# Performance work log

Hardware: AMD Instinct MI355X
Metric: run time of the kernel (lower is better)

## Reference

```python
import jax, jax.numpy as jnp
import numpy as np

BS, TS, H = 16, 2048, 1024
MT_LEN = TS // 2  # static split point; matches first_sentence_mask built in setup_inputs
SCALE = 1.0 / float(np.sqrt(H))
NEG = -10000.0


def masked_average(x, mask):
    # x: (bs, ts, h), mask: (bs, ts) -> (bs, h)
    m = mask[..., None].astype(x.dtype)
    return (x * m).sum(1) / m.sum(1)


def setup_inputs() -> dict:
    key = jax.random.key(0)
    ks = jax.random.split(key, 8)
    hidden_states = jax.random.normal(ks[0], (BS, TS, H), jnp.float32)
    embeddings = jax.random.normal(ks[1], (BS, TS, H), jnp.float32)
    attention_mask = jnp.ones((BS, TS), jnp.int32)
    first_sentence_mask = jnp.concatenate(
        [jnp.ones((BS, MT_LEN), jnp.int32), jnp.zeros((BS, TS - MT_LEN), jnp.int32)], axis=1)
    first_piece_mask = jnp.ones((BS, TS), jnp.int32)  # unused (aggregation='none')
    s = 1.0 / float(np.sqrt(H))
    Wq = jax.random.normal(ks[2], (H, H), jnp.float32) * s
    bq = jnp.zeros((H,), jnp.float32)
    Wk = jax.random.normal(ks[3], (H, H), jnp.float32) * s
    bk = jnp.zeros((H,), jnp.float32)
    Wv = jax.random.normal(ks[4], (H, H), jnp.float32) * s
    bv = jnp.zeros((H,), jnp.float32)
    return dict(hidden_states=hidden_states, embeddings=embeddings,
                attention_mask=attention_mask, first_sentence_mask=first_sentence_mask,
                first_piece_mask=first_piece_mask,
                Wq=Wq, bq=bq, Wk=Wk, bk=bk, Wv=Wv, bv=bv)


def reference(hidden_states, embeddings, attention_mask, first_sentence_mask,
              first_piece_mask, Wq, bq, Wk, bk, Wv, bv):
    # alpha_merge < 0, squared_attn=False, kv_rep='embeddings', alpha=1.0 (softmax)
    kv_rep = embeddings
    hidden_states_avg = masked_average(hidden_states, attention_mask)   # (bs, h)
    q = hidden_states_avg @ Wq.T + bq                                   # (bs, h)
    k = kv_rep @ Wk.T + bk                                              # (bs, ts, h)
    v = kv_rep @ Wv.T + bv                                              # (bs, ts, h)
    scores = jnp.einsum('bh,bth->bt', q, k) * SCALE                     # (bs, ts)
    scores = jnp.where(attention_mask.astype(bool), scores, NEG)
    probas = jax.nn.softmax(scores, axis=-1)                            # (bs, ts)
    combined_summary = jnp.einsum('bt,bth->bh', probas, v)              # (bs, h)
    # separate_mt_and_src on probas (static split at MT_LEN)
    mt_mask = attention_mask[:, :MT_LEN] * first_sentence_mask[:, :MT_LEN]
    src_mask = attention_mask[:, MT_LEN:] * (1 - first_sentence_mask[:, MT_LEN:])
    mt_probas = probas[:, :MT_LEN] * mt_mask.astype(probas.dtype)
    src_probas = probas[:, MT_LEN:] * src_mask.astype(probas.dtype)
    return combined_summary, mt_probas, src_probas
```

## Files before the change

### kernel.cpp

```cpp
#include <hip/hip_runtime.h>

#define BS 16
#define TS 2048
#define H 1024
#define MT_LEN 1024
#define NCHUNK 64
#define CHUNK_T (TS / NCHUNK)
#define SCALE 0.03125f
#define NEG -10000.0f

__global__ __launch_bounds__(256)
void k1_hidden_partial(const float* __restrict__ hs,
                       const int* __restrict__ am,
                       float* __restrict__ pA) {
    const int c = blockIdx.x, b = blockIdx.y;
    const int tid = threadIdx.x;
    const int h4 = tid * 4;
    __shared__ float ms[CHUNK_T];
    if (tid < CHUNK_T) ms[tid] = (float)am[b * TS + c * CHUNK_T + tid];
    __syncthreads();
    const float* base = hs + ((size_t)(b * TS + c * CHUNK_T)) * H + h4;
    float4 acc = {0.f, 0.f, 0.f, 0.f};
#pragma unroll 4
    for (int t = 0; t < CHUNK_T; ++t) {
        float m = ms[t];
        float4 v = *(const float4*)(base + (size_t)t * H);
        acc.x += m * v.x; acc.y += m * v.y; acc.z += m * v.z; acc.w += m * v.w;
    }
    *(float4*)(pA + ((size_t)(b * NCHUNK + c)) * H + h4) = acc;
}

__global__ __launch_bounds__(256)
void k3_q(const float* __restrict__ pA, const int* __restrict__ am,
          const float* __restrict__ Wq, const float* __restrict__ bq,
          float* __restrict__ q) {
    const int ic = blockIdx.x, b = blockIdx.y;
    const int tid = threadIdx.x;
    __shared__ float avs[H];
    __shared__ float red[256];
    int s = 0;
    for (int t = tid; t < TS; t += 256) s += am[b * TS + t];
    red[tid] = (float)s;
    __syncthreads();
    for (int o = 128; o > 0; o >>= 1) { if (tid < o) red[tid] += red[tid + o]; __syncthreads(); }
    const float inv = 1.0f / red[0];
    const int h4 = tid * 4;
    float4 acc = {0.f, 0.f, 0.f, 0.f};
    for (int c = 0; c < NCHUNK; ++c) {
        float4 v = *(const float4*)(pA + ((size_t)(b * NCHUNK + c)) * H + h4);
        acc.x += v.x; acc.y += v.y; acc.z += v.z; acc.w += v.w;
    }
    avs[h4] = acc.x * inv; avs[h4 + 1] = acc.y * inv;
    avs[h4 + 2] = acc.z * inv; avs[h4 + 3] = acc.w * inv;
    __syncthreads();
    const int i = ic * 256 + tid;
    const float* row = Wq + (size_t)i * H;
    float a = 0.f;
    for (int j = 0; j < H; j += 4) {
        float4 w = *(const float4*)(row + j);
        a += w.x * avs[j] + w.y * avs[j + 1] + w.z * avs[j + 2] + w.w * avs[j + 3];
    }
    q[b * H + i] = a + bq[i];
}

__global__ __launch_bounds__(256)
void k4_qk(const float* __restrict__ q, const float* __restrict__ Wk,
           const float* __restrict__ bk, float* __restrict__ qk,
           float* __restrict__ qbk) {
    const int jc = blockIdx.x, b = blockIdx.y;
    const int tid = threadIdx.x;
    __shared__ float qs[H];
    for (int i = tid; i < H; i += 256) qs[i] = q[b * H + i];
    __syncthreads();
    const int j = jc * 256 + tid;
    float acc = 0.f;
    for (int i = 0; i < H; ++i) acc += qs[i] * Wk[(size_t)i * H + j];
    qk[b * H + j] = acc;
    if (jc == 0) {
        __shared__ float red[256];
        float s = 0.f;
        for (int i = tid; i < H; i += 256) s += qs[i] * bk[i];
        red[tid] = s;
        __syncthreads();
        for (int o = 128; o > 0; o >>= 1) { if (tid < o) red[tid] += red[tid + o]; __syncthreads(); }
        if (tid == 0) qbk[b] = red[0];
    }
}

__global__ __launch_bounds__(256)
void k5_scores(const float* __restrict__ emb, const int* __restrict__ am,
               const float* __restrict__ qk, const float* __restrict__ qbk,
               float* __restrict__ scores) {
    const int c = blockIdx.x, b = blockIdx.y;
    const int tid = threadIdx.x;
    const int wave = tid >> 6, lane = tid & 63;
    __shared__ float qks[H];
    for (int j = tid; j < H; j += 256) qks[j] = qk[b * H + j];
    __syncthreads();
    const float qb = qbk[b];
    const int tbase = c * CHUNK_T + wave * (CHUNK_T / 4);
    for (int tt = 0; tt < CHUNK_T / 4; ++tt) {
        const int t = tbase + tt;
        const float* e = emb + ((size_t)(b * TS + t)) * H;
        float acc = 0.f;
#pragma unroll
        for (int u = 0; u < 4; ++u) {
            const int j = lane * 4 + u * 256;
            float4 v = *(const float4*)(e + j);
            acc += v.x * qks[j] + v.y * qks[j + 1] + v.z * qks[j + 2] + v.w * qks[j + 3];
        }
#pragma unroll
        for (int o = 32; o > 0; o >>= 1) acc += __shfl_xor(acc, o);
        if (lane == 0) {
            scores[b * TS + t] = (am[b * TS + t] != 0) ? (acc + qb) * SCALE : NEG;
        }
    }
}

__global__ __launch_bounds__(256)
void k6_softmax(const float* __restrict__ scores, const int* __restrict__ am,
                const int* __restrict__ fs, float* __restrict__ probas,
                float* __restrict__ out) {
    const int b = blockIdx.x;
    const int tid = threadIdx.x;
    __shared__ float red[256];
    float local[8];
    float mx = -3.4e38f;
#pragma unroll
    for (int u = 0; u < 8; ++u) {
        local[u] = scores[b * TS + tid + u * 256];
        mx = fmaxf(mx, local[u]);
    }
    red[tid] = mx;
    __syncthreads();
    for (int o = 128; o > 0; o >>= 1) { if (tid < o) red[tid] = fmaxf(red[tid], red[tid + o]); __syncthreads(); }
    mx = red[0];
    __syncthreads();
    float sum = 0.f;
#pragma unroll
    for (int u = 0; u < 8; ++u) { local[u] = __expf(local[u] - mx); sum += local[u]; }
    red[tid] = sum;
    __syncthreads();
    for (int o = 128; o > 0; o >>= 1) { if (tid < o) red[tid] += red[tid + o]; __syncthreads(); }
    const float inv = 1.0f / red[0];
#pragma unroll
    for (int u = 0; u < 8; ++u) {
        const int t = tid + u * 256;
        const float p = local[u] * inv;
        probas[b * TS + t] = p;
        const int a = am[b * TS + t];
        const int f = fs[b * TS + t];
        if (t < MT_LEN)
            out[BS * H + b * MT_LEN + t] = p * (float)(a * f);
        else
            out[BS * H + BS * MT_LEN + b * (TS - MT_LEN) + (t - MT_LEN)] = p * (float)(a * (1 - f));
    }
}

__global__ __launch_bounds__(256)
void k7_wemb(const float* __restrict__ emb, const float* __restrict__ probas,
             float* __restrict__ pC) {
    const int c = blockIdx.x, b = blockIdx.y;
    const int tid = threadIdx.x;
    __shared__ float ps[CHUNK_T];
    if (tid < CHUNK_T) ps[tid] = probas[b * TS + c * CHUNK_T + tid];
    __syncthreads();
    const int h4 = tid * 4;
    const float* base = emb + ((size_t)(b * TS + c * CHUNK_T)) * H + h4;
    float4 acc = {0.f, 0.f, 0.f, 0.f};
#pragma unroll 4
    for (int t = 0; t < CHUNK_T; ++t) {
        const float p = ps[t];
        float4 v = *(const float4*)(base + (size_t)t * H);
        acc.x += p * v.x; acc.y += p * v.y; acc.z += p * v.z; acc.w += p * v.w;
    }
    *(float4*)(pC + ((size_t)(b * NCHUNK + c)) * H + h4) = acc;
}

__global__ __launch_bounds__(256)
void k8_combined(const float* __restrict__ pC, const float* __restrict__ Wv,
                 const float* __restrict__ bv, float* __restrict__ out) {
    const int ic = blockIdx.x, b = blockIdx.y;
    const int tid = threadIdx.x;
    __shared__ float es[H];
    const int h4 = tid * 4;
    float4 acc = {0.f, 0.f, 0.f, 0.f};
    for (int c = 0; c < NCHUNK; ++c) {
        float4 v = *(const float4*)(pC + ((size_t)(b * NCHUNK + c)) * H + h4);
        acc.x += v.x; acc.y += v.y; acc.z += v.z; acc.w += v.w;
    }
    *(float4*)(&es[h4]) = acc;
    __syncthreads();
    const int i = ic * 256 + tid;
    const float* row = Wv + (size_t)i * H;
    float a = 0.f;
    for (int j = 0; j < H; j += 4) {
        float4 w = *(const float4*)(row + j);
        a += w.x * es[j] + w.y * es[j + 1] + w.z * es[j + 2] + w.w * es[j + 3];
    }
    out[b * H + i] = a + bv[i];
}

extern "C" void kernel_launch(void* const* d_in, const int* in_sizes, int n_in,
                              void* d_out, int out_size, void* d_ws, size_t ws_size,
                              hipStream_t stream) {
    const float* hs  = (const float*)d_in[0];
    const float* emb = (const float*)d_in[1];
    const int*   am  = (const int*)d_in[2];
    const int*   fs  = (const int*)d_in[3];
    const float* Wq  = (const float*)d_in[5];
    const float* bq  = (const float*)d_in[6];
    const float* Wk  = (const float*)d_in[7];
    const float* bk  = (const float*)d_in[8];
    const float* Wv  = (const float*)d_in[9];
    const float* bv  = (const float*)d_in[10];
    float* out = (float*)d_out;
    float* ws  = (float*)d_ws;

    float* pA     = ws;
    float* q      = ws + 1048576;
    float* qk     = ws + 1064960;
    float* qbk    = ws + 1081344;
    float* scores = ws + 1082368;
    float* probas = ws + 1115136;
    float* pC     = ws + 1147904;

    const dim3 gridBC(NCHUNK, BS);
    k1_hidden_partial<<<gridBC, 256, 0, stream>>>(hs, am, pA);
    k3_q<<<dim3(4, BS), 256, 0, stream>>>(pA, am, Wq, bq, q);
    k4_qk<<<dim3(4, BS), 256, 0, stream>>>(q, Wk, bk, qk, qbk);
    k5_scores<<<gridBC, 256, 0, stream>>>(emb, am, qk, qbk, scores);
    k6_softmax<<<BS, 256, 0, stream>>>(scores, am, fs, probas, out);
    k7_wemb<<<gridBC, 256, 0, stream>>>(emb, probas, pC);
    k8_combined<<<dim3(4, BS), 256, 0, stream>>>(pC, Wv, bv, out);
}
```

Baseline: 440.1 us.

## Fuse scores and weighted-sum via chunked online softmax, reshape GEMV kernels

Merges score computation and the probability-weighted embedding sum into one kernel, using per-chunk max and normaliser values combined later in a split-softmax reduction. Each chunk's embeddings are then read while still hot in cache instead of in a second full pass over the 128 MB embeddings tensor. The Wq and Wv GEMVs are restructured to one wavefront per output row with coalesced reads and many more blocks, and the Wk GEMV is split along the input dimension for coalesced float4 reads. The cost is extra small launches, a larger workspace and recomputing exp for the probability outputs.

```diff
diff --git a/kernel.cpp b/kernel.cpp
--- a/kernel.cpp
+++ b/kernel.cpp
@@ -23,7 +23,7 @@
     float4 acc = {0.f, 0.f, 0.f, 0.f};
 #pragma unroll 4
     for (int t = 0; t < CHUNK_T; ++t) {
-        float m = ms[t];
+        const float m = ms[t];
         float4 v = *(const float4*)(base + (size_t)t * H);
         acc.x += m * v.x; acc.y += m * v.y; acc.z += m * v.z; acc.w += m * v.w;
     }
@@ -31,12 +31,10 @@
 }
 
 __global__ __launch_bounds__(256)
-void k3_q(const float* __restrict__ pA, const int* __restrict__ am,
-          const float* __restrict__ Wq, const float* __restrict__ bq,
-          float* __restrict__ q) {
-    const int ic = blockIdx.x, b = blockIdx.y;
-    const int tid = threadIdx.x;
-    __shared__ float avs[H];
+void k2_avg(const float* __restrict__ pA, const int* __restrict__ am,
+            float* __restrict__ avg) {
+    const int b = blockIdx.x;
+    const int tid = threadIdx.x;
     __shared__ float red[256];
     int s = 0;
     for (int t = tid; t < TS; t += 256) s += am[b * TS + t];
@@ -50,104 +48,163 @@
         float4 v = *(const float4*)(pA + ((size_t)(b * NCHUNK + c)) * H + h4);
         acc.x += v.x; acc.y += v.y; acc.z += v.z; acc.w += v.w;
     }
-    avs[h4] = acc.x * inv; avs[h4 + 1] = acc.y * inv;
-    avs[h4 + 2] = acc.z * inv; avs[h4 + 3] = acc.w * inv;
-    __syncthreads();
-    const int i = ic * 256 + tid;
+    acc.x *= inv; acc.y *= inv; acc.z *= inv; acc.w *= inv;
+    *(float4*)(avg + (size_t)b * H + h4) = acc;
+}
+
+__global__ __launch_bounds__(256)
+void k3_q(const float* __restrict__ avg, const float* __restrict__ Wq,
+          const float* __restrict__ bq, float* __restrict__ q) {
+    const int b = blockIdx.y;
+    const int tid = threadIdx.x;
+    __shared__ float avs[H];
+    *(float4*)(&avs[tid * 4]) = *(const float4*)(avg + (size_t)b * H + tid * 4);
+    __syncthreads();
+    const int wave = tid >> 6, lane = tid & 63;
+    const int i = blockIdx.x * 4 + wave;
     const float* row = Wq + (size_t)i * H;
-    float a = 0.f;
-    for (int j = 0; j < H; j += 4) {
+    float acc = 0.f;
+#pragma unroll
+    for (int u = 0; u < 4; ++u) {
+        const int j = u * 256 + lane * 4;
         float4 w = *(const float4*)(row + j);
-        a += w.x * avs[j] + w.y * avs[j + 1] + w.z * avs[j + 2] + w.w * avs[j + 3];
-    }
-    q[b * H + i] = a + bq[i];
-}
-
-__global__ __launch_bounds__(256)
-void k4_qk(const float* __restrict__ q, const float* __restrict__ Wk,
-           const float* __restrict__ bk, float* __restrict__ qk,
-           float* __restrict__ qbk) {
-    const int jc = blockIdx.x, b = blockIdx.y;
-    const int tid = threadIdx.x;
-    __shared__ float qs[H];
-    for (int i = tid; i < H; i += 256) qs[i] = q[b * H + i];
-    __syncthreads();
-    const int j = jc * 256 + tid;
-    float acc = 0.f;
-    for (int i = 0; i < H; ++i) acc += qs[i] * Wk[(size_t)i * H + j];
-    qk[b * H + j] = acc;
-    if (jc == 0) {
-        __shared__ float red[256];
-        float s = 0.f;
-        for (int i = tid; i < H; i += 256) s += qs[i] * bk[i];
-        red[tid] = s;
-        __syncthreads();
-        for (int o = 128; o > 0; o >>= 1) { if (tid < o) red[tid] += red[tid + o]; __syncthreads(); }
-        if (tid == 0) qbk[b] = red[0];
-    }
-}
-
-__global__ __launch_bounds__(256)
-void k5_scores(const float* __restrict__ emb, const int* __restrict__ am,
-               const float* __restrict__ qk, const float* __restrict__ qbk,
-               float* __restrict__ scores) {
+        float4 a = *(const float4*)(&avs[j]);
+        acc += w.x * a.x + w.y * a.y + w.z * a.z + w.w * a.w;
+    }
+#pragma unroll
+    for (int o = 32; o > 0; o >>= 1) acc += __shfl_xor(acc, o);
+    if (lane == 0) q[b * H + i] = acc + bq[i];
+}
+
+__global__ __launch_bounds__(256)
+void k4_qkp(const float* __restrict__ q, const float* __restrict__ Wk,
+            const float* __restrict__ bk, float* __restrict__ qk_p,
+            float* __restrict__ qbk_p) {
+    const int ic = blockIdx.x, b = blockIdx.y;
+    const int tid = threadIdx.x;
+    __shared__ float qs[256];
+    __shared__ float red[256];
+    qs[tid] = q[b * H + ic * 256 + tid];
+    __syncthreads();
+    const int j = tid * 4;
+    float4 acc = {0.f, 0.f, 0.f, 0.f};
+#pragma unroll 8
+    for (int ii = 0; ii < 256; ++ii) {
+        const float s = qs[ii];
+        float4 w = *(const float4*)(Wk + ((size_t)(ic * 256 + ii)) * H + j);
+        acc.x += s * w.x; acc.y += s * w.y; acc.z += s * w.z; acc.w += s * w.w;
+    }
+    *(float4*)(qk_p + ((size_t)(ic * BS + b)) * H + j) = acc;
+    red[tid] = qs[tid] * bk[ic * 256 + tid];
+    __syncthreads();
+    for (int o = 128; o > 0; o >>= 1) { if (tid < o) red[tid] += red[tid + o]; __syncthreads(); }
+    if (tid == 0) qbk_p[ic * BS + b] = red[0];
+}
+
+__global__ __launch_bounds__(256)
+void k5_fused(const float* __restrict__ emb, const int* __restrict__ am,
+              const float* __restrict__ qk_p, const float* __restrict__ qbk_p,
+              float* __restrict__ scores, float* __restrict__ mc_arr,
+              float* __restrict__ zc_arr, float* __restrict__ e_c) {
     const int c = blockIdx.x, b = blockIdx.y;
     const int tid = threadIdx.x;
+    __shared__ float qks[H];
+    __shared__ float sbuf[CHUNK_T];
+    __shared__ float wbuf[CHUNK_T];
+    {
+        const int j = tid * 4;
+        float4 a = {0.f, 0.f, 0.f, 0.f};
+#pragma unroll
+        for (int ic = 0; ic < 4; ++ic) {
+            float4 v = *(const float4*)(qk_p + ((size_t)(ic * BS + b)) * H + j);
+            a.x += v.x; a.y += v.y; a.z += v.z; a.w += v.w;
+        }
+        *(float4*)(&qks[j]) = a;
+    }
+    const float qb = qbk_p[0 * BS + b] + qbk_p[1 * BS + b] + qbk_p[2 * BS + b] + qbk_p[3 * BS + b];
+    __syncthreads();
     const int wave = tid >> 6, lane = tid & 63;
-    __shared__ float qks[H];
-    for (int j = tid; j < H; j += 256) qks[j] = qk[b * H + j];
-    __syncthreads();
-    const float qb = qbk[b];
-    const int tbase = c * CHUNK_T + wave * (CHUNK_T / 4);
-    for (int tt = 0; tt < CHUNK_T / 4; ++tt) {
-        const int t = tbase + tt;
+    for (int tt = 0; tt < 8; ++tt) {
+        const int tl = wave * 8 + tt;
+        const int t = c * CHUNK_T + tl;
         const float* e = emb + ((size_t)(b * TS + t)) * H;
         float acc = 0.f;
 #pragma unroll
         for (int u = 0; u < 4; ++u) {
-            const int j = lane * 4 + u * 256;
+            const int j = u * 256 + lane * 4;
             float4 v = *(const float4*)(e + j);
-            acc += v.x * qks[j] + v.y * qks[j + 1] + v.z * qks[j + 2] + v.w * qks[j + 3];
+            float4 a = *(const float4*)(&qks[j]);
+            acc += v.x * a.x + v.y * a.y + v.z * a.z + v.w * a.w;
         }
 #pragma unroll
         for (int o = 32; o > 0; o >>= 1) acc += __shfl_xor(acc, o);
         if (lane == 0) {
-            scores[b * TS + t] = (am[b * TS + t] != 0) ? (acc + qb) * SCALE : NEG;
+            const float sc = (am[b * TS + t] != 0) ? (acc + qb) * SCALE : NEG;
+            scores[b * TS + t] = sc;
+            sbuf[tl] = sc;
         }
     }
-}
-
-__global__ __launch_bounds__(256)
-void k6_softmax(const float* __restrict__ scores, const int* __restrict__ am,
-                const int* __restrict__ fs, float* __restrict__ probas,
-                float* __restrict__ out) {
+    __syncthreads();
+    float mc = -3.4e38f;
+#pragma unroll
+    for (int tl = 0; tl < CHUNK_T; ++tl) mc = fmaxf(mc, sbuf[tl]);
+    if (tid < CHUNK_T) wbuf[tid] = __expf(sbuf[tid] - mc);
+    __syncthreads();
+    float zc = 0.f;
+#pragma unroll
+    for (int tl = 0; tl < CHUNK_T; ++tl) zc += wbuf[tl];
+    const int h4 = tid * 4;
+    const float* base = emb + ((size_t)(b * TS + c * CHUNK_T)) * H + h4;
+    float4 acc = {0.f, 0.f, 0.f, 0.f};
+#pragma unroll 4
+    for (int t = 0; t < CHUNK_T; ++t) {
+        const float p = wbuf[t];
+        float4 v = *(const float4*)(base + (size_t)t * H);
+        acc.x += p * v.x; acc.y += p * v.y; acc.z += p * v.z; acc.w += p * v.w;
+    }
+    *(float4*)(e_c + ((size_t)(b * NCHUNK + c)) * H + h4) = acc;
+    if (tid == 0) { mc_arr[b * NCHUNK + c] = mc; zc_arr[b * NCHUNK + c] = zc; }
+}
+
+__global__ __launch_bounds__(256)
+void k6_combine(const float* __restrict__ mc_arr, const float* __restrict__ zc_arr,
+                const float* __restrict__ e_c, float* __restrict__ e_comb,
+                float* __restrict__ mz) {
     const int b = blockIdx.x;
     const int tid = threadIdx.x;
-    __shared__ float red[256];
-    float local[8];
-    float mx = -3.4e38f;
-#pragma unroll
-    for (int u = 0; u < 8; ++u) {
-        local[u] = scores[b * TS + tid + u * 256];
-        mx = fmaxf(mx, local[u]);
-    }
-    red[tid] = mx;
-    __syncthreads();
-    for (int o = 128; o > 0; o >>= 1) { if (tid < o) red[tid] = fmaxf(red[tid], red[tid + o]); __syncthreads(); }
-    mx = red[0];
-    __syncthreads();
-    float sum = 0.f;
-#pragma unroll
-    for (int u = 0; u < 8; ++u) { local[u] = __expf(local[u] - mx); sum += local[u]; }
-    red[tid] = sum;
-    __syncthreads();
-    for (int o = 128; o > 0; o >>= 1) { if (tid < o) red[tid] += red[tid + o]; __syncthreads(); }
-    const float inv = 1.0f / red[0];
+    __shared__ float mcs[NCHUNK], zcs[NCHUNK], scs[NCHUNK];
+    if (tid < NCHUNK) { mcs[tid] = mc_arr[b * NCHUNK + tid]; zcs[tid] = zc_arr[b * NCHUNK + tid]; }
+    __syncthreads();
+    float m = -3.4e38f;
+    for (int c = 0; c < NCHUNK; ++c) m = fmaxf(m, mcs[c]);
+    float Z = 0.f;
+    for (int c = 0; c < NCHUNK; ++c) Z += zcs[c] * __expf(mcs[c] - m);
+    if (tid < NCHUNK) scs[tid] = __expf(mcs[tid] - m);
+    __syncthreads();
+    const float invZ = 1.0f / Z;
+    const int h4 = tid * 4;
+    float4 acc = {0.f, 0.f, 0.f, 0.f};
+    for (int c = 0; c < NCHUNK; ++c) {
+        const float s = scs[c];
+        float4 v = *(const float4*)(e_c + ((size_t)(b * NCHUNK + c)) * H + h4);
+        acc.x += s * v.x; acc.y += s * v.y; acc.z += s * v.z; acc.w += s * v.w;
+    }
+    acc.x *= invZ; acc.y *= invZ; acc.z *= invZ; acc.w *= invZ;
+    *(float4*)(e_comb + (size_t)b * H + h4) = acc;
+    if (tid == 0) { mz[b * 2] = m; mz[b * 2 + 1] = invZ; }
+}
+
+__global__ __launch_bounds__(256)
+void k7_probas(const float* __restrict__ scores, const float* __restrict__ mz,
+               const int* __restrict__ am, const int* __restrict__ fs,
+               float* __restrict__ out) {
+    const int b = blockIdx.x;
+    const int tid = threadIdx.x;
+    const float m = mz[b * 2], invZ = mz[b * 2 + 1];
 #pragma unroll
     for (int u = 0; u < 8; ++u) {
         const int t = tid + u * 256;
-        const float p = local[u] * inv;
-        probas[b * TS + t] = p;
+        const float p = __expf(scores[b * TS + t] - m) * invZ;
         const int a = am[b * TS + t];
         const int f = fs[b * TS + t];
         if (t < MT_LEN)
@@ -158,47 +215,27 @@
 }
 
 __global__ __launch_bounds__(256)
-void k7_wemb(const float* __restrict__ emb, const float* __restrict__ probas,
-             float* __restrict__ pC) {
-    const int c = blockIdx.x, b = blockIdx.y;
-    const int tid = threadIdx.x;
-    __shared__ float ps[CHUNK_T];
-    if (tid < CHUNK_T) ps[tid] = probas[b * TS + c * CHUNK_T + tid];
-    __syncthreads();
-    const int h4 = tid * 4;
-    const float* base = emb + ((size_t)(b * TS + c * CHUNK_T)) * H + h4;
-    float4 acc = {0.f, 0.f, 0.f, 0.f};
-#pragma unroll 4
-    for (int t = 0; t < CHUNK_T; ++t) {
-        const float p = ps[t];
-        float4 v = *(const float4*)(base + (size_t)t * H);
-        acc.x += p * v.x; acc.y += p * v.y; acc.z += p * v.z; acc.w += p * v.w;
-    }
-    *(float4*)(pC + ((size_t)(b * NCHUNK + c)) * H + h4) = acc;
-}
-
-__global__ __launch_bounds__(256)
-void k8_combined(const float* __restrict__ pC, const float* __restrict__ Wv,
-                 const float* __restrict__ bv, float* __restrict__ out) {
-    const int ic = blockIdx.x, b = blockIdx.y;
+void k8_out(const float* __restrict__ e_comb, const float* __restrict__ Wv,
+            const float* __restrict__ bv, float* __restrict__ out) {
+    const int b = blockIdx.y;
     const int tid = threadIdx.x;
     __shared__ float es[H];
-    const int h4 = tid * 4;
-    float4 acc = {0.f, 0.f, 0.f, 0.f};
-    for (int c = 0; c < NCHUNK; ++c) {
-        float4 v = *(const float4*)(pC + ((size_t)(b * NCHUNK + c)) * H + h4);
-        acc.x += v.x; acc.y += v.y; acc.z += v.z; acc.w += v.w;
-    }
-    *(float4*)(&es[h4]) = acc;
-    __syncthreads();
-    const int i = ic * 256 + tid;
+    *(float4*)(&es[tid * 4]) = *(const float4*)(e_comb + (size_t)b * H + tid * 4);
+    __syncthreads();
+    const int wave = tid >> 6, lane = tid & 63;
+    const int i = blockIdx.x * 4 + wave;
     const float* row = Wv + (size_t)i * H;
-    float a = 0.f;
-    for (int j = 0; j < H; j += 4) {
+    float acc = 0.f;
+#pragma unroll
+    for (int u = 0; u < 4; ++u) {
+        const int j = u * 256 + lane * 4;
         float4 w = *(const float4*)(row + j);
-        a += w.x * es[j] + w.y * es[j + 1] + w.z * es[j + 2] + w.w * es[j + 3];
-    }
-    out[b * H + i] = a + bv[i];
+        float4 a = *(const float4*)(&es[j]);
+        acc += w.x * a.x + w.y * a.y + w.z * a.z + w.w * a.w;
+    }
+#pragma unroll
+    for (int o = 32; o > 0; o >>= 1) acc += __shfl_xor(acc, o);
+    if (lane == 0) out[b * H + i] = acc + bv[i];
 }
 
 extern "C" void kernel_launch(void* const* d_in, const int* in_sizes, int n_in,
@@ -218,19 +255,24 @@
     float* ws  = (float*)d_ws;
 
     float* pA     = ws;
-    float* q      = ws + 1048576;
-    float* qk     = ws + 1064960;
-    float* qbk    = ws + 1081344;
-    float* scores = ws + 1082368;
-    float* probas = ws + 1115136;
-    float* pC     = ws + 1147904;
-
-    const dim3 gridBC(NCHUNK, BS);
-    k1_hidden_partial<<<gridBC, 256, 0, stream>>>(hs, am, pA);
-    k3_q<<<dim3(4, BS), 256, 0, stream>>>(pA, am, Wq, bq, q);
-    k4_qk<<<dim3(4, BS), 256, 0, stream>>>(q, Wk, bk, qk, qbk);
-    k5_scores<<<gridBC, 256, 0, stream>>>(emb, am, qk, qbk, scores);
-    k6_softmax<<<BS, 256, 0, stream>>>(scores, am, fs, probas, out);
-    k7_wemb<<<gridBC, 256, 0, stream>>>(emb, probas, pC);
-    k8_combined<<<dim3(4, BS), 256, 0, stream>>>(pC, Wv, bv, out);
-}
+    float* avg    = ws + 1048576;
+    float* q      = ws + 1064960;
+    float* qk_p   = ws + 1081344;
+    float* qbk_p  = ws + 1146880;
+    float* scores = ws + 1147136;
+    float* mc_arr = ws + 1179904;
+    float* zc_arr = ws + 1180928;
+    float* e_c    = ws + 1181952;
+    float* mz     = ws + 2230528;
+    float* e_comb = ws + 2230784;
+
+    k1_hidden_partial<<<dim3(NCHUNK, BS), 256, 0, stream>>>(hs, am, pA);
+    k2_avg<<<BS, 256, 0, stream>>>(pA, am, avg);
+    k3_q<<<dim3(H / 4, BS), 256, 0, stream>>>(avg, Wq, bq, q);
+    k4_qkp<<<dim3(4, BS), 256, 0, stream>>>(q, Wk, bk, qk_p, qbk_p);
+    k5_fused<<<dim3(NCHUNK, BS), 256, 0, stream>>>(emb, am, qk_p, qbk_p,
+                                                   scores, mc_arr, zc_arr, e_c);
+    k6_combine<<<BS, 256, 0, stream>>>(mc_arr, zc_arr, e_c, e_comb, mz);
+    k7_probas<<<BS, 256, 0, stream>>>(scores, mz, am, fs, out);
+    k8_out<<<dim3(H / 4, BS), 256, 0, stream>>>(e_comb, Wv, bv, out);
+}
```

Measured after the change: 361.6 us. 1.22x faster.
